# Kernel optimization log

Hardware: AMD Instinct MI355X
Metric: run time of the kernel (lower is better)

The kernel has to match this reference:

```python
import jax, jax.numpy as jnp
import numpy as np

T = 10.0           # distillation temperature (init arg T)
LOSS_WEIGHT = 1.0  # module-level loss_weight (init arg)
EPS_STD = 1e-07
EPS_RATIO = 1e-08

ROWS, BINS = 1048576, 17  # (4*N, n+1), n = 16


def setup_inputs() -> dict:
    key = jax.random.key(0)
    k1, k2, k3 = jax.random.split(key, 3)
    pred = jax.random.normal(k1, (ROWS, BINS), dtype=jnp.float32)
    soft_label = jax.random.normal(k2, (ROWS, BINS), dtype=jnp.float32)
    weight = jax.random.uniform(k3, (ROWS,), dtype=jnp.float32)
    return {"pred": pred, "soft_label": soft_label, "weight": weight}


def _normalize(logit):
    # torch .std() is unbiased (ddof=1)
    mean = jnp.mean(logit, axis=-1, keepdims=True)
    stdv = jnp.std(logit, axis=-1, keepdims=True, ddof=1)
    return (logit - mean) / (EPS_STD + stdv)


def reference(pred, soft_label, weight):
    soft = jax.lax.stop_gradient(soft_label)  # detach_target=True

    # kd_loss_ls with logit_stand=True
    ls = _normalize(pred)
    lt = _normalize(soft)
    log_p_student = jax.nn.log_softmax(ls / T, axis=1)
    log_p_teacher = jax.nn.log_softmax(lt / T, axis=1)
    p_teacher = jnp.exp(log_p_teacher)
    # F.kl_div(log_pred, target, 'none') = target * (log(target) - log_pred)
    loss_ls = jnp.mean(jnp.sum(p_teacher * (log_p_teacher - log_p_student), axis=1)) * (T * T)

    # sum_distributions_loop on target = softmax(soft_label) -- batched full conv1d
    target = jax.nn.softmax(soft, axis=1)            # (4N, bins)
    n_rows, bins = target.shape
    N = n_rows // 4
    t = target.reshape(N, 4, bins)
    top, bottom, left, right = t[:, 0], t[:, 1], t[:, 2], t[:, 3]
    # pad+flip+conv1d in torch == true full convolution, length 2*bins-1 = 2n+1
    conv_full = jax.vmap(lambda a, b: jnp.convolve(a, b, mode='full'))
    sum_lr = conv_full(left, right)                   # (N, 2n+1)
    sum_tb = conv_full(top, bottom)                   # (N, 2n+1)
    target_ratio = sum_lr / (sum_tb + EPS_RATIO)

    # weighted_loss wrapper: loss * weight, then 'mean' reduction; outer * loss_weight
    loss = LOSS_WEIGHT * jnp.mean(loss_ls * weight)
    return loss, target_ratio
```

## Files before the change

### kernel.cpp

```cpp
#include <hip/hip_runtime.h>

#define ROWS 1048576
#define BINS 17
#define RPB 128
#define NBLK (ROWS / RPB)
#define NPART (2 * NBLK)
#define GPB (RPB / 4)
#define CONV_N 33
#define L2E 1.442695040888963f
#define LN2 0.6931471805599453f

template <bool PART>
__global__ __launch_bounds__(128, 8) void kd_main(
    const float* __restrict__ pred,
    const float* __restrict__ soft,
    const float* __restrict__ weight,
    float* __restrict__ out,
    float* __restrict__ ws)
{
    __shared__ float sA[RPB * BINS + RPB];
    float* sI = sA + RPB * BINS;
    const int tid = threadIdx.x;

    const long long rowbase = ((long long)blockIdx.x * RPB + tid) * BINS;
    const float* px = pred + rowbase;
    const float* py = soft + rowbase;
    float x[BINS], y[BINS];
#pragma unroll
    for (int j = 0; j < BINS; ++j) x[j] = px[j];
#pragma unroll
    for (int j = 0; j < BINS; ++j) y[j] = py[j];
    const float w = weight[blockIdx.x * RPB + tid];

    float sx = 0.f, sy = 0.f, sxx = 0.f, syy = 0.f;
    float xmx = -1e30f, ymx = -1e30f;
#pragma unroll
    for (int j = 0; j < BINS; ++j) {
        sx += x[j]; sxx = fmaf(x[j], x[j], sxx); xmx = fmaxf(xmx, x[j]);
        sy += y[j]; syy = fmaf(y[j], y[j], syy); ymx = fmaxf(ymx, y[j]);
    }
    const float mx = sx * (1.0f / BINS);
    const float my = sy * (1.0f / BINS);
    const float vx = fmaxf(fmaf(-sx, mx, sxx), 0.f) * (1.0f / (BINS - 1));
    const float vy = fmaxf(fmaf(-sy, my, syy), 0.f) * (1.0f / (BINS - 1));
    const float sxl = (0.1f * L2E) *
        __builtin_amdgcn_rcpf(1e-7f + __builtin_amdgcn_sqrtf(vx));
    const float syl = (0.1f * L2E) *
        __builtin_amdgcn_rcpf(1e-7f + __builtin_amdgcn_sqrtf(vy));
    const float cA = -xmx * sxl;
    const float cB = -ymx * syl;
    const float cT = -ymx * L2E;

    float sea = 0.f, seb = 0.f, ts = 0.f, sdb = 0.f;
#pragma unroll
    for (int j = 0; j < BINS; ++j) {
        const float aj = fmaf(x[j], sxl, cA);
        const float bj = fmaf(y[j], syl, cB);
        const float ea = exp2f(aj);
        const float eb = exp2f(bj);
        const float tv = exp2f(fmaf(y[j], L2E, cT));
        sea += ea; seb += eb; ts += tv;
        sdb = fmaf(eb, bj - aj, sdb);
        sA[tid * BINS + j] = tv;
    }
    const float kl = LN2 * (sdb * __builtin_amdgcn_rcpf(seb)
                            + (__log2f(sea) - __log2f(seb)));
    sI[tid] = __builtin_amdgcn_rcpf(ts);

    float k2 = kl, w2 = w;
#pragma unroll
    for (int off = 32; off >= 1; off >>= 1) {
        k2 += __shfl_down(k2, off, 64);
        w2 += __shfl_down(w2, off, 64);
    }
    if ((tid & 63) == 0) {
        const int wv = tid >> 6;
        if (PART) {
            ws[2 * blockIdx.x + wv]         = k2;
            ws[NPART + 2 * blockIdx.x + wv] = w2;
        } else {
            atomicAdd(&ws[0], k2);
            atomicAdd(&ws[1], w2);
        }
    }

    __syncthreads();

    float* sR = sA;

    if (tid < 64) {
        const int g = tid >> 1;
        const int R = 4 * g + ((tid & 1) ? 0 : 2);
        const float s0 = sI[R], s1 = sI[R + 1];
        float f[2 * BINS];
        const float2* pr = reinterpret_cast<const float2*>(&sA[R * BINS]);
#pragma unroll
        for (int i = 0; i < BINS; ++i) {
            const float2 v = pr[i];
            f[2 * i]     = v.x * (2 * i     < BINS ? s0 : s1);
            f[2 * i + 1] = v.y * (2 * i + 1 < BINS ? s0 : s1);
        }
        float accv[CONV_N];
#pragma unroll
        for (int j = 0; j < CONV_N; ++j) accv[j] = 0.f;
#pragma unroll
        for (int k = 0; k < BINS; ++k)
#pragma unroll
            for (int m = 0; m < BINS; ++m)
                accv[k + m] = fmaf(f[k], f[BINS + m], accv[k + m]);

#pragma unroll
        for (int j = 0; j < CONV_N; ++j) {
            const float o = __shfl_down(accv[j], 1, 64);
            if ((tid & 1) == 0)
                sR[g * CONV_N + j] = accv[j] *
                    __builtin_amdgcn_rcpf(o + 1e-8f);
        }
    }
    __syncthreads();

    const long long ob = 1 + (long long)blockIdx.x * (GPB * CONV_N);
#pragma unroll
    for (int i = 0; i < 8; ++i)
        out[ob + i * RPB + tid] = sR[i * RPB + tid];
    if (tid < 32) out[ob + 1024 + tid] = sR[1024 + tid];
}

template <bool PART>
__global__ __launch_bounds__(1024) void kd_reduce(
    const float* __restrict__ ws, float* __restrict__ out)
{
    if (!PART) {
        if (threadIdx.x == 0)
            out[0] = 100.0f * (ws[0] * (1.0f / ROWS)) * (ws[1] * (1.0f / ROWS));
        return;
    }
    __shared__ float red[32];
    const int tid = threadIdx.x;
    const float4* k4 = reinterpret_cast<const float4*>(ws);
    const float4* w4 = reinterpret_cast<const float4*>(ws + NPART);
    float ks = 0.f, wsum = 0.f;
#pragma unroll
    for (int i = 0; i < 4; ++i) {
        const float4 a = k4[i * 1024 + tid];
        const float4 b = w4[i * 1024 + tid];
        ks += (a.x + a.y) + (a.z + a.w);
        wsum += (b.x + b.y) + (b.z + b.w);
    }
#pragma unroll
    for (int off = 32; off >= 1; off >>= 1) {
        ks += __shfl_down(ks, off, 64);
        wsum += __shfl_down(wsum, off, 64);
    }
    if ((tid & 63) == 0) {
        red[(tid >> 6) * 2 + 0] = ks;
        red[(tid >> 6) * 2 + 1] = wsum;
    }
    __syncthreads();
    if (tid == 0) {
        float K = 0.f, W = 0.f;
#pragma unroll
        for (int i = 0; i < 16; ++i) { K += red[2 * i]; W += red[2 * i + 1]; }
        out[0] = 100.0f * (K * (1.0f / ROWS)) * (W * (1.0f / ROWS));
    }
}

extern "C" void kernel_launch(void* const* d_in, const int* in_sizes, int n_in,
                              void* d_out, int out_size, void* d_ws, size_t ws_size,
                              hipStream_t stream)
{
    const float* pred   = (const float*)d_in[0];
    const float* soft   = (const float*)d_in[1];
    const float* weight = (const float*)d_in[2];
    float* out = (float*)d_out;
    float* ws  = (float*)d_ws;

    if (ws_size >= (size_t)(2 * NPART) * sizeof(float)) {
        kd_main<true><<<NBLK, RPB, 0, stream>>>(pred, soft, weight, out, ws);
        kd_reduce<true><<<1, 1024, 0, stream>>>(ws, out);
    } else {
        hipMemsetAsync(ws, 0, 2 * sizeof(float), stream);
        kd_main<false><<<NBLK, RPB, 0, stream>>>(pred, soft, weight, out, ws);
        kd_reduce<false><<<1, 1024, 0, stream>>>(ws, out);
    }
}
```

Before: 181.8 us.

## Compute convolutions in registers across all lanes using DPP quad swaps

Each thread now normalises its own teacher softmax row in registers. Instead of staging rows in LDS for half the block, every lane convolves its row with its quad partner's row, fetched with a DPP lane swap, and a second DPP swap pairs the left-right result with the top-bottom result for the ratio. This removes the LDS staging and the first barrier, and spreads the convolution across both waves instead of leaving one idle. The cost is that each convolution is computed twice. The launch bound is relaxed to 4 blocks per SIMD to allow the extra register pressure.

```diff
diff --git a/kernel.cpp b/kernel.cpp
--- a/kernel.cpp
+++ b/kernel.cpp
@@ -10,16 +10,25 @@
 #define L2E 1.442695040888963f
 #define LN2 0.6931471805599453f
 
+
+__device__ __forceinline__ float qx1(float v) {
+    return __int_as_float(__builtin_amdgcn_update_dpp(
+        0, __float_as_int(v), 0xB1, 0xF, 0xF, true));
+}
+__device__ __forceinline__ float qx2(float v) {
+    return __int_as_float(__builtin_amdgcn_update_dpp(
+        0, __float_as_int(v), 0x4E, 0xF, 0xF, true));
+}
+
 template <bool PART>
-__global__ __launch_bounds__(128, 8) void kd_main(
+__global__ __launch_bounds__(128, 4) void kd_main(
     const float* __restrict__ pred,
     const float* __restrict__ soft,
     const float* __restrict__ weight,
     float* __restrict__ out,
     float* __restrict__ ws)
 {
-    __shared__ float sA[RPB * BINS + RPB];
-    float* sI = sA + RPB * BINS;
+    __shared__ float sR[GPB * CONV_N];
     const int tid = threadIdx.x;
 
     const long long rowbase = ((long long)blockIdx.x * RPB + tid) * BINS;
@@ -51,6 +60,7 @@
     const float cB = -ymx * syl;
     const float cT = -ymx * L2E;
 
+    float et[BINS];
     float sea = 0.f, seb = 0.f, ts = 0.f, sdb = 0.f;
 #pragma unroll
     for (int j = 0; j < BINS; ++j) {
@@ -61,11 +71,13 @@
         const float tv = exp2f(fmaf(y[j], L2E, cT));
         sea += ea; seb += eb; ts += tv;
         sdb = fmaf(eb, bj - aj, sdb);
-        sA[tid * BINS + j] = tv;
+        et[j] = tv;
     }
     const float kl = LN2 * (sdb * __builtin_amdgcn_rcpf(seb)
                             + (__log2f(sea) - __log2f(seb)));
-    sI[tid] = __builtin_amdgcn_rcpf(ts);
+    const float invts = __builtin_amdgcn_rcpf(ts);
+#pragma unroll
+    for (int j = 0; j < BINS; ++j) et[j] *= invts;
 
     float k2 = kl, w2 = w;
 #pragma unroll
@@ -84,38 +96,26 @@
         }
     }
 
-    __syncthreads();
+    float f2[BINS];
+#pragma unroll
+    for (int j = 0; j < BINS; ++j) f2[j] = qx1(et[j]);
 
-    float* sR = sA;
+    float acc[CONV_N];
+#pragma unroll
+    for (int j = 0; j < CONV_N; ++j) acc[j] = 0.f;
+#pragma unroll
+    for (int k = 0; k < BINS; ++k)
+#pragma unroll
+        for (int m = 0; m < BINS; ++m)
+            acc[k + m] = fmaf(et[k], f2[m], acc[k + m]);
 
-    if (tid < 64) {
-        const int g = tid >> 1;
-        const int R = 4 * g + ((tid & 1) ? 0 : 2);
-        const float s0 = sI[R], s1 = sI[R + 1];
-        float f[2 * BINS];
-        const float2* pr = reinterpret_cast<const float2*>(&sA[R * BINS]);
+    const int r = tid & 3;
+    const int g = tid >> 2;
 #pragma unroll
-        for (int i = 0; i < BINS; ++i) {
-            const float2 v = pr[i];
-            f[2 * i]     = v.x * (2 * i     < BINS ? s0 : s1);
-            f[2 * i + 1] = v.y * (2 * i + 1 < BINS ? s0 : s1);
-        }
-        float accv[CONV_N];
-#pragma unroll
-        for (int j = 0; j < CONV_N; ++j) accv[j] = 0.f;
-#pragma unroll
-        for (int k = 0; k < BINS; ++k)
-#pragma unroll
-            for (int m = 0; m < BINS; ++m)
-                accv[k + m] = fmaf(f[k], f[BINS + m], accv[k + m]);
-
-#pragma unroll
-        for (int j = 0; j < CONV_N; ++j) {
-            const float o = __shfl_down(accv[j], 1, 64);
-            if ((tid & 1) == 0)
-                sR[g * CONV_N + j] = accv[j] *
-                    __builtin_amdgcn_rcpf(o + 1e-8f);
-        }
+    for (int j = 0; j < CONV_N; ++j) {
+        const float o = qx2(acc[j]);
+        if (r == (j < BINS ? 0 : 1))
+            sR[g * CONV_N + j] = o * __builtin_amdgcn_rcpf(acc[j] + 1e-8f);
     }
     __syncthreads();
 
```

New measurement: 182.4 us. Within noise of the previous version (+0.3%).
